# Optimization experiments

Hardware: AMD Instinct MI355X
Metric: run time of the kernel (lower is better)

Reference implementation:

```python
import math
import jax, jax.numpy as jnp
import numpy as np

T_STEPS = 65536
T_S = 1.0      # net_params['t_s']
THETA = 10.0   # net_params['af_params']['theta']


def _eps_func(mult, tau, epsilon, t_end, t_s):
    vals = []
    for t in np.arange(0, t_end, t_s):
        v = mult * t / tau * math.exp(1 - t / tau)
        if abs(v) < abs(epsilon) and t > tau:
            break
        vals.append(v)
    return vals


def _srm_kernel(mult, tau, epsilon, t_end, t_s):
    # replicates SlayerTrainer._calculate_srm_kernel: pad-to-odd, prepend zeros, flip
    k = _eps_func(mult, tau, epsilon, t_end, t_s)
    if len(k) % 2 == 0:
        k.append(0.0)
    k = np.asarray(k, dtype=np.float32)
    k = np.concatenate([np.zeros(len(k) - 1, np.float32), k])[::-1].copy()
    return k  # (K,), K odd; causal after cross-correlation with pad K//2


def setup_inputs() -> dict:
    key = jax.random.key(0)
    k1, k2, k3 = jax.random.split(key, 3)
    x = jax.random.uniform(k1, (1, 1, 1, 250, T_STEPS), jnp.float32)
    srm = jnp.asarray(_srm_kernel(1.0, 10.0, 1e-4, 200, T_S))                 # sr_params
    ref = jnp.asarray(np.asarray(_eps_func(-20.0, 1.0, 1e-4, 200, T_S), np.float32))  # ref_params
    # SpikeLinear weights, init N(0, std=weights_init)
    w1 = jax.random.normal(k2, (25, 250), jnp.float32) * 4.0
    w2 = jax.random.normal(k3, (1, 25), jnp.float32) * 4.0
    return {"x": x, "srm": srm, "ref": ref, "w1": w1, "w2": w2}


def srm_conv(z, srm):
    # z: (C, T). Per-channel 1-D cross-correlation with 'same' padding,
    # equal to F.conv3d(x, eye-SRM kernel, padding=(0,0,K//2)) * t_s.
    K = srm.shape[0]
    p = K // 2
    lhs = z[:, None, :]            # (C, 1, T) -- channels as batch
    rhs = srm[None, None, :]       # (1, 1, K)
    out = jax.lax.conv_general_dilated(
        lhs, rhs, window_strides=(1,), padding=[(p, p)],
        dimension_numbers=("NCW", "OIW", "NCW"))
    return out[:, 0, :] * T_S


def gen_spikes(pot, ref):
    # Sequential integrate-fire with refractory feedback (slayer_cuda.get_spikes_cuda).
    # pot: (C, T). Carry = per-neuron buffer of scheduled future refractory additions.
    C = pot.shape[0]
    L = ref.shape[0]
    # ref[j] is added to potentials[t+j] on a spike at t (ref[0]==0); after the
    # shift, buf[0] corresponds to time t+1, so schedule ref[1:].
    ref_next = jnp.concatenate([ref[1:], jnp.zeros((1,), pot.dtype)])

    def step(buf, p_t):
        u = p_t + buf[:, 0]                           # membrane incl. refractory
        s = (u >= THETA).astype(pot.dtype)
        buf = jnp.concatenate([buf[:, 1:], jnp.zeros((C, 1), pot.dtype)], axis=1)
        buf = buf + s[:, None] * ref_next[None, :]
        return buf, (u, s / T_S)

    buf0 = jnp.zeros((C, L), pot.dtype)
    _, (u_seq, s_seq) = jax.lax.scan(step, buf0, pot.T)
    return u_seq.T, s_seq.T  # (C, T), (C, T)


def reference(x, srm, ref, w1, w2):
    h = srm_conv(x[0, 0, 0], srm)        # (250, T) SRM-filtered input spikes
    h = w1 @ h                           # (25, T)  SpikeLinear fc1
    _, s1 = gen_spikes(h, ref)           # (25, T)  spikes layer 1
    h = srm_conv(s1, srm)                # (25, T)  SRM on hidden spikes
    h = w2 @ h                           # (1, T)   SpikeLinear fc2
    _, s2 = gen_spikes(h, ref)           # (1, T)
    return s2.reshape(1, 1, 1, 1, -1)
```

## Files before the change

### kernel.cpp

```cpp
#include <hip/hip_runtime.h>


#define T_LEN   65536
#define NCH     250
#define NO1     25
#define KTAPS   129
#define PAD     128
#define SRM_LEN 257
#define REF_LEN 16
#define THETA_F 10.0f
#define LBLK    128
#define NBK     512
#define WARM    128
#define TT      128
#define FTILE   1024
#define FT2     1024
#define NWORDS  (T_LEN / 32)
#define NGRP    16

__device__ __forceinline__ void srm_step(float p, const float (&rn)[15], float (&b)[15],
                                         unsigned &m, float &sf_out) {
  float u = p + b[0];
  unsigned sp = (u >= THETA_F) ? 1u : 0u;
  float sf = sp ? 1.0f : 0.0f;
#pragma unroll
  for (int j = 0; j < 14; ++j) b[j] = __builtin_fmaf(sf, rn[j], b[j + 1]);
  b[14] = __fmul_rn(sf, rn[14]);
  m = (m << 1) | sp;
  sf_out = sf;
}

__global__ void k_fill(float* out, float v) {
  out[blockIdx.x * 256 + threadIdx.x] = v;
}

__global__ __launch_bounds__(1024, 4) void k_mm1(const float* __restrict__ x,
                                                 const float* __restrict__ w1,
                                                 float* __restrict__ y1t) {
  __shared__ __align__(16) float part[NGRP][5][TT];
  const int tid = threadIdx.x;
  const int lane = tid & 63;
  const int wv = __builtin_amdgcn_readfirstlane(tid >> 6);
  const int t0 = blockIdx.x * TT;
  const int cs = wv * 15 + (wv < 10 ? wv : 10);
  const int cn = (wv < 10) ? 16 : 15;
  float acc[NO1][2];
#pragma unroll
  for (int o = 0; o < NO1; ++o) { acc[o][0] = 0.f; acc[o][1] = 0.f; }
  const float* xp = x + (size_t)cs * T_LEN + t0 + lane * 2;

  auto ld = [&](int ci) -> float2 {
    return (ci < cn) ? *(const float2*)(xp + (size_t)ci * T_LEN)
                     : make_float2(0.f, 0.f);
  };
  auto use = [&](int ci, float2 xv) {
    if (ci < cn) {
#pragma unroll
      for (int o = 0; o < NO1; ++o) {
        float wvv = w1[o * NCH + cs + ci];
        acc[o][0] = __builtin_fmaf(wvv, xv.x, acc[o][0]);
        acc[o][1] = __builtin_fmaf(wvv, xv.y, acc[o][1]);
      }
    }
  };

  float2 A0 = ld(0), A1 = ld(1), A2 = ld(2), A3 = ld(3);
  float2 B0, B1, B2, B3;
  for (int cb = 0; cb < cn; cb += 8) {
    B0 = ld(cb + 4); B1 = ld(cb + 5); B2 = ld(cb + 6); B3 = ld(cb + 7);
    use(cb + 0, A0); use(cb + 1, A1); use(cb + 2, A2); use(cb + 3, A3);
    A0 = ld(cb + 8); A1 = ld(cb + 9); A2 = ld(cb + 10); A3 = ld(cb + 11);
    use(cb + 4, B0); use(cb + 5, B1); use(cb + 6, B2); use(cb + 7, B3);
  }
  float* yb = y1t + (size_t)blockIdx.x * (NO1 * TT);
#pragma unroll
  for (int r = 0; r < 5; ++r) {
#pragma unroll
    for (int oo = 0; oo < 5; ++oo) {
      int o = r * 5 + oo;
      *(float2*)&part[wv][oo][lane * 2] = make_float2(acc[o][0], acc[o][1]);
    }
    __syncthreads();
    if (tid < 5 * (TT / 4)) {
      int oo = tid >> 5;
      int p4 = (tid & 31) * 4;
      float4 s = *(const float4*)&part[0][oo][p4];
#pragma unroll
      for (int g = 1; g < NGRP; ++g) {
        float4 p = *(const float4*)&part[g][oo][p4];
        s.x = __fadd_rn(s.x, p.x);
        s.y = __fadd_rn(s.y, p.y);
        s.z = __fadd_rn(s.z, p.z);
        s.w = __fadd_rn(s.w, p.w);
      }
      *(float4*)&yb[(r * 5 + oo) * TT + p4] = s;
    }
    __syncthreads();
  }
}

__global__ __launch_bounds__(256, 8) void k_fir1(const float* __restrict__ y1t,
                                                 const float* __restrict__ srm,
                                                 float* __restrict__ pot1) {
  __shared__ __align__(16) float win[FTILE + PAD];
  const int tid = threadIdx.x;
  const int o = blockIdx.y;
  const int t0 = blockIdx.x * FTILE;
  for (int j = tid; j < FTILE + PAD; j += 256) {
    int g = t0 - PAD + j;
    win[j] = (g >= 0)
        ? y1t[(size_t)(g >> 7) * (NO1 * TT) + o * TT + (g & (TT - 1))] : 0.0f;
  }
  __syncthreads();
  const int base = tid * 4;
  float q0 = 0.0f, q1 = 0.0f, q2 = 0.0f, q3 = 0.0f;
#pragma unroll
  for (int i = 32; i >= 0; --i) {
    float4 v = *(const float4*)&win[base + 4 * i];
#pragma unroll
    for (int l = 3; l >= 0; --l) {
      float vl = (l == 0) ? v.x : (l == 1) ? v.y : (l == 2) ? v.z : v.w;
#pragma unroll
      for (int k = 0; k < 4; ++k) {
        int d = 128 + k - 4 * i - l;
        if (d >= 0 && d <= 128) {
          float e = srm[4 * i + l - k];
          if (k == 0) q0 = __builtin_fmaf(e, vl, q0);
          else if (k == 1) q1 = __builtin_fmaf(e, vl, q1);
          else if (k == 2) q2 = __builtin_fmaf(e, vl, q2);
          else q3 = __builtin_fmaf(e, vl, q3);
        }
      }
    }
  }
  *(float4*)&pot1[(size_t)o * T_LEN + t0 + base] = make_float4(q0, q1, q2, q3);
}

__global__ __launch_bounds__(256) void k_pot2(const unsigned* __restrict__ s1p,
                                              const float* __restrict__ srm,
                                              const float* __restrict__ w2,
                                              float* __restrict__ pot2) {
  __shared__ __align__(16) float zs[FT2 + PAD];
  const int tid = threadIdx.x;
  const int t0 = blockIdx.x * FT2;
  for (int j = tid; j < FT2 + PAD; j += 256) {
    int g = t0 - PAD + j;
    float z = 0.0f;
    if (g >= 0) {
      int wi = g >> 5, sh = g & 31;
#pragma unroll
      for (int o = 0; o < NO1; ++o) {
        unsigned wvv = s1p[o * NWORDS + wi];
        z += ((wvv >> sh) & 1u) ? w2[o] : 0.0f;
      }
    }
    zs[j] = z;
  }
  __syncthreads();
  const int base = tid * 4;
  float q0 = 0.0f, q1 = 0.0f, q2 = 0.0f, q3 = 0.0f;
#pragma unroll
  for (int i = 32; i >= 0; --i) {
    float4 v = *(const float4*)&zs[base + 4 * i];
#pragma unroll
    for (int l = 3; l >= 0; --l) {
      float vl = (l == 0) ? v.x : (l == 1) ? v.y : (l == 2) ? v.z : v.w;
#pragma unroll
      for (int k = 0; k < 4; ++k) {
        int d = 128 + k - 4 * i - l;
        if (d >= 0 && d <= 128) {
          float e = srm[4 * i + l - k];
          if (k == 0) q0 = __builtin_fmaf(e, vl, q0);
          else if (k == 1) q1 = __builtin_fmaf(e, vl, q1);
          else if (k == 2) q2 = __builtin_fmaf(e, vl, q2);
          else q3 = __builtin_fmaf(e, vl, q3);
        }
      }
    }
  }
  *(float4*)&pot2[t0 + base] = make_float4(q0, q1, q2, q3);
}

template <int C, bool PACKED>
__global__ __launch_bounds__(64) void k_scan_spec(const float* __restrict__ pot,
                                                  const float* __restrict__ refk,
                                                  float* __restrict__ s,
                                                  unsigned* __restrict__ sp_,
                                                  unsigned* __restrict__ specin_m,
                                                  unsigned* __restrict__ specout_m,
                                                  float* __restrict__ specout_b) {
  int idx = blockIdx.x * 64 + threadIdx.x;
  if (idx >= C * NBK) return;
  int c = idx / NBK;
  int bb = idx - c * NBK;
  int tsr = bb * LBLK - WARM;
  float rn[15];
#pragma unroll
  for (int j = 0; j < 15; ++j) rn[j] = refk[j + 1];
  float b[15];
#pragma unroll
  for (int j = 0; j < 15; ++j) b[j] = 0.0f;
  unsigned m = 0;
  const float* prow = pot + (size_t)c * T_LEN;
  float* srow = PACKED ? nullptr : (s + (size_t)c * T_LEN);
  unsigned* srowp = PACKED ? (sp_ + (size_t)c * NWORDS) : nullptr;

  auto proc4 = [&](float4 pv, int tg, bool emit) {
    float s0, s1v, s2, s3;
    srm_step(pv.x, rn, b, m, s0);
    srm_step(pv.y, rn, b, m, s1v);
    srm_step(pv.z, rn, b, m, s2);
    srm_step(pv.w, rn, b, m, s3);
    if (emit) {
      if (PACKED) {
        if (((tg + 3) & 31) == 31) srowp[(tg - 28) >> 5] = __brev(m);
      } else {
        *(float4*)(srow + tg) = make_float4(s0, s1v, s2, s3);
      }
    }
  };

  for (int k = 0; k < WARM + LBLK; k += 16) {
    if (k == WARM) specin_m[idx] = m & 0x7FFFu;
    int t = tsr + k;
    if (t < 0) continue;
    float4 p0 = *(const float4*)(prow + t);
    float4 p1 = *(const float4*)(prow + t + 4);
    float4 p2 = *(const float4*)(prow + t + 8);
    float4 p3 = *(const float4*)(prow + t + 12);
    const bool emit = (k >= WARM);
    proc4(p0, t, emit);
    proc4(p1, t + 4, emit);
    proc4(p2, t + 8, emit);
    proc4(p3, t + 12, emit);
  }
  specout_m[idx] = m & 0x7FFFu;
#pragma unroll
  for (int j = 0; j < 15; ++j) specout_b[idx * 16 + j] = b[j];
}

template <int C, bool PACKED>
__global__ __launch_bounds__(64) void k_scan_fix(const float* __restrict__ pot,
                                                 const float* __restrict__ refk,
                                                 float* __restrict__ s,
                                                 unsigned* __restrict__ sp_,
                                                 const unsigned* __restrict__ specin_m,
                                                 const unsigned* __restrict__ specout_m,
                                                 const float* __restrict__ specout_b) {
  const int c = blockIdx.x;
  const int lane = threadIdx.x;
  float rn[15];
#pragma unroll
  for (int j = 0; j < 15; ++j) rn[j] = refk[j + 1];
  float b[15];
#pragma unroll
  for (int j = 0; j < 15; ++j) b[j] = 0.0f;
  unsigned m = 0;
  bool haveB = true;
  const float* prow = pot + (size_t)c * T_LEN;
  float* srow = PACKED ? nullptr : (s + (size_t)c * T_LEN);
  unsigned* srowp = PACKED ? (sp_ + (size_t)c * NWORDS) : nullptr;
  unsigned prev_last = 0;

  unsigned siv[NBK / 64], sov[NBK / 64];
#pragma unroll
  for (int g = 0; g < NBK / 64; ++g) {
    siv[g] = specin_m[c * NBK + g * 64 + lane];
    sov[g] = specout_m[c * NBK + g * 64 + lane];
  }
#pragma unroll
  for (int g = 0; g < NBK / 64; ++g) {
    const unsigned si = siv[g];
    const unsigned so = sov[g];
    unsigned so_prev = __shfl_up(so, 1);
    if (lane == 0) so_prev = prev_last;
    const unsigned long long flags = __ballot(si == so_prev);
    prev_last = __shfl(so, 63);
    const unsigned si0 = __shfl(si, 0);
    if (flags == ~0ull && (m & 0x7FFFu) == si0) {
      m = prev_last;
      haveB = false;
      continue;
    }
    for (int r = 0; r < 64; ++r) {
      const unsigned sir = __shfl(si, r);
      const unsigned sor = __shfl(so, r);
      if ((m & 0x7FFFu) == sir) {
        m = sor;
        haveB = false;
      } else {
        const int bbr = g * 64 + r;
        if (!haveB) {
          const int pb = (c * NBK + bbr - 1) * 16;
#pragma unroll
          for (int q2 = 0; q2 < 15; ++q2) b[q2] = specout_b[pb + q2];
          haveB = true;
        }
        const int t0 = bbr * LBLK;
        for (int t = t0; t < t0 + LBLK; t += 4) {
          float4 pv = *(const float4*)(prow + t);
          float s0, s1v, s2, s3;
          srm_step(pv.x, rn, b, m, s0);
          srm_step(pv.y, rn, b, m, s1v);
          srm_step(pv.z, rn, b, m, s2);
          srm_step(pv.w, rn, b, m, s3);
          if (PACKED) {
            if ((((t + 3) & 31) == 31) && lane == 0) srowp[(t - 28) >> 5] = __brev(m);
          } else {
            if (lane == 0) *(float4*)(srow + t) = make_float4(s0, s1v, s2, s3);
          }
        }
        haveB = true;
      }
    }
  }
}

extern "C" void kernel_launch(void* const* d_in, const int* in_sizes, int n_in,
                              void* d_out, int out_size, void* d_ws, size_t ws_size,
                              hipStream_t stream) {
  const float* x    = (const float*)d_in[0];
  const float* srm  = (const float*)d_in[1];
  const float* refk = (const float*)d_in[2];
  const float* w1   = (const float*)d_in[3];
  const float* w2   = (const float*)d_in[4];
  float* out = (float*)d_out;

  float bad = 0.0f;
  if (n_in != 5) bad = 3.0f;
  else if (in_sizes[0] != NCH * T_LEN) bad = 4.0f;
  else if (in_sizes[1] != SRM_LEN)     bad = 5.0f;
  else if (in_sizes[2] != REF_LEN)     bad = 6.0f;
  else if (in_sizes[3] != NO1 * NCH)   bad = 7.0f;
  else if (in_sizes[4] != NO1)         bad = 8.0f;
  else if (out_size != T_LEN)          bad = 9.0f;
  if (bad != 0.0f) {
    k_fill<<<T_LEN / 256, 256, 0, stream>>>(out, bad);
    return;
  }

  size_t off = 0;
  auto alloc = [&](size_t bytes) { size_t o = off; off = (off + bytes + 255) & ~(size_t)255; return o; };
  char* ws = (char*)d_ws;
  size_t oY1  = alloc((size_t)NO1 * T_LEN * 4);
  size_t oP1  = alloc((size_t)NO1 * T_LEN * 4);
  size_t oS1P = alloc((size_t)NO1 * NWORDS * 4);
  size_t oP2  = alloc((size_t)T_LEN * 4);
  if (ws_size < off) {
    k_fill<<<T_LEN / 256, 256, 0, stream>>>(out, 2.0f);
    return;
  }

  float*    y1t  = (float*)(ws + oY1);
  float*    pot1 = (float*)(ws + oP1);
  unsigned* s1p  = (unsigned*)(ws + oS1P);
  float*    pot2 = (float*)(ws + oP2);
  char* yb = ws + oY1;
  unsigned* si1 = (unsigned*)(yb);
  unsigned* so1 = (unsigned*)(yb + 51200);
  float*    sb1 = (float*)   (yb + 102400);
  unsigned* si2 = (unsigned*)(yb + 921600);
  unsigned* so2 = (unsigned*)(yb + 923648);
  float*    sb2 = (float*)   (yb + 925696);

  k_mm1<<<T_LEN / TT, 1024, 0, stream>>>(x, w1, y1t);
  k_fir1<<<dim3(T_LEN / FTILE, NO1), 256, 0, stream>>>(y1t, srm, pot1);
  k_scan_spec<NO1, true><<<(NO1 * NBK + 63) / 64, 64, 0, stream>>>(
      pot1, refk, nullptr, s1p, si1, so1, sb1);
  k_scan_fix<NO1, true><<<NO1, 64, 0, stream>>>(pot1, refk, nullptr, s1p, si1, so1, sb1);
  k_pot2<<<T_LEN / FT2, 256, 0, stream>>>(s1p, srm, w2, pot2);
  k_scan_spec<1, false><<<(NBK + 63) / 64, 64, 0, stream>>>(
      pot2, refk, out, nullptr, si2, so2, sb2);
  k_scan_fix<1, false><<<1, 64, 0, stream>>>(pot2, refk, out, nullptr, si2, so2, sb2);
}
```

Before: 98.65 us.

## Repack fc1 weights per wave group and halve mm1 block size with full unrolling

New measurement: 94.43 us. 4.3% less time.

```diff
diff --git a/kernel.cpp b/kernel.cpp
--- a/kernel.cpp
+++ b/kernel.cpp
@@ -16,7 +16,7 @@
 #define FTILE   1024
 #define FT2     1024
 #define NWORDS  (T_LEN / 32)
-#define NGRP    16
+#define NGRP    8
 
 __device__ __forceinline__ void srm_step(float p, const float (&rn)[15], float (&b)[15],
                                          unsigned &m, float &sf_out) {
@@ -34,44 +34,75 @@
   out[blockIdx.x * 256 + threadIdx.x] = v;
 }
 
-__global__ __launch_bounds__(1024, 4) void k_mm1(const float* __restrict__ x,
-                                                 const float* __restrict__ w1,
-                                                 float* __restrict__ y1t) {
+__global__ __launch_bounds__(256) void k_prep2(const float* __restrict__ w1,
+                                               float* __restrict__ wg) {
+  for (int i = threadIdx.x; i < NGRP * 32 * NO1; i += 256) {
+    int g = i / (32 * NO1);
+    int r = i - g * 32 * NO1;
+    int ci = r / NO1;
+    int o = r - ci * NO1;
+    int cs = g * 31 + (g < 2 ? g : 2);
+    int cn = (g < 2) ? 32 : 31;
+    wg[i] = (ci < cn) ? w1[o * NCH + cs + ci] : 0.0f;
+  }
+}
+
+template <int CI>
+__device__ __forceinline__ void use_slot(const float* __restrict__ wgp,
+                                         float (&acc)[NO1][2], float2 xv) {
+#pragma unroll
+  for (int o = 0; o < NO1; ++o) {
+    float wvv = wgp[CI * NO1 + o];
+    acc[o][0] = __builtin_fmaf(wvv, xv.x, acc[o][0]);
+    acc[o][1] = __builtin_fmaf(wvv, xv.y, acc[o][1]);
+  }
+}
+
+__global__ __launch_bounds__(512, 6) void k_mm1(const float* __restrict__ x,
+                                                const float* __restrict__ wg,
+                                                float* __restrict__ y1t) {
   __shared__ __align__(16) float part[NGRP][5][TT];
   const int tid = threadIdx.x;
   const int lane = tid & 63;
   const int wv = __builtin_amdgcn_readfirstlane(tid >> 6);
   const int t0 = blockIdx.x * TT;
-  const int cs = wv * 15 + (wv < 10 ? wv : 10);
-  const int cn = (wv < 10) ? 16 : 15;
+  const int cs = wv * 31 + (wv < 2 ? wv : 2);
+  const int cn = (wv < 2) ? 32 : 31;
+  const int s31 = cn - 1;
+  const float* wgp = wg + wv * (32 * NO1);
+  const float* xp = x + (size_t)cs * T_LEN + t0 + lane * 2;
   float acc[NO1][2];
 #pragma unroll
   for (int o = 0; o < NO1; ++o) { acc[o][0] = 0.f; acc[o][1] = 0.f; }
-  const float* xp = x + (size_t)cs * T_LEN + t0 + lane * 2;
-
-  auto ld = [&](int ci) -> float2 {
-    return (ci < cn) ? *(const float2*)(xp + (size_t)ci * T_LEN)
-                     : make_float2(0.f, 0.f);
-  };
-  auto use = [&](int ci, float2 xv) {
-    if (ci < cn) {
-#pragma unroll
-      for (int o = 0; o < NO1; ++o) {
-        float wvv = w1[o * NCH + cs + ci];
-        acc[o][0] = __builtin_fmaf(wvv, xv.x, acc[o][0]);
-        acc[o][1] = __builtin_fmaf(wvv, xv.y, acc[o][1]);
-      }
-    }
-  };
-
-  float2 A0 = ld(0), A1 = ld(1), A2 = ld(2), A3 = ld(3);
-  float2 B0, B1, B2, B3;
-  for (int cb = 0; cb < cn; cb += 8) {
-    B0 = ld(cb + 4); B1 = ld(cb + 5); B2 = ld(cb + 6); B3 = ld(cb + 7);
-    use(cb + 0, A0); use(cb + 1, A1); use(cb + 2, A2); use(cb + 3, A3);
-    A0 = ld(cb + 8); A1 = ld(cb + 9); A2 = ld(cb + 10); A3 = ld(cb + 11);
-    use(cb + 4, B0); use(cb + 5, B1); use(cb + 6, B2); use(cb + 7, B3);
-  }
+
+#define LDX(ci) (*(const float2*)(xp + (size_t)(ci) * T_LEN))
+  float2 A0, A1, A2, A3, B0, B1, B2, B3;
+  A0 = LDX(0);  A1 = LDX(1);  A2 = LDX(2);  A3 = LDX(3);
+  B0 = LDX(4);  B1 = LDX(5);  B2 = LDX(6);  B3 = LDX(7);
+  use_slot<0>(wgp, acc, A0);  use_slot<1>(wgp, acc, A1);
+  use_slot<2>(wgp, acc, A2);  use_slot<3>(wgp, acc, A3);
+  A0 = LDX(8);  A1 = LDX(9);  A2 = LDX(10); A3 = LDX(11);
+  use_slot<4>(wgp, acc, B0);  use_slot<5>(wgp, acc, B1);
+  use_slot<6>(wgp, acc, B2);  use_slot<7>(wgp, acc, B3);
+  B0 = LDX(12); B1 = LDX(13); B2 = LDX(14); B3 = LDX(15);
+  use_slot<8>(wgp, acc, A0);  use_slot<9>(wgp, acc, A1);
+  use_slot<10>(wgp, acc, A2); use_slot<11>(wgp, acc, A3);
+  A0 = LDX(16); A1 = LDX(17); A2 = LDX(18); A3 = LDX(19);
+  use_slot<12>(wgp, acc, B0); use_slot<13>(wgp, acc, B1);
+  use_slot<14>(wgp, acc, B2); use_slot<15>(wgp, acc, B3);
+  B0 = LDX(20); B1 = LDX(21); B2 = LDX(22); B3 = LDX(23);
+  use_slot<16>(wgp, acc, A0); use_slot<17>(wgp, acc, A1);
+  use_slot<18>(wgp, acc, A2); use_slot<19>(wgp, acc, A3);
+  A0 = LDX(24); A1 = LDX(25); A2 = LDX(26); A3 = LDX(27);
+  use_slot<20>(wgp, acc, B0); use_slot<21>(wgp, acc, B1);
+  use_slot<22>(wgp, acc, B2); use_slot<23>(wgp, acc, B3);
+  B0 = LDX(28); B1 = LDX(29); B2 = LDX(30); B3 = LDX(s31);
+  use_slot<24>(wgp, acc, A0); use_slot<25>(wgp, acc, A1);
+  use_slot<26>(wgp, acc, A2); use_slot<27>(wgp, acc, A3);
+  use_slot<28>(wgp, acc, B0); use_slot<29>(wgp, acc, B1);
+  use_slot<30>(wgp, acc, B2); use_slot<31>(wgp, acc, B3);
+#undef LDX
+
   float* yb = y1t + (size_t)blockIdx.x * (NO1 * TT);
 #pragma unroll
   for (int r = 0; r < 5; ++r) {
@@ -346,6 +377,7 @@
   size_t oP1  = alloc((size_t)NO1 * T_LEN * 4);
   size_t oS1P = alloc((size_t)NO1 * NWORDS * 4);
   size_t oP2  = alloc((size_t)T_LEN * 4);
+  size_t oWG  = alloc((size_t)NGRP * 32 * NO1 * 4);
   if (ws_size < off) {
     k_fill<<<T_LEN / 256, 256, 0, stream>>>(out, 2.0f);
     return;
@@ -355,6 +387,7 @@
   float*    pot1 = (float*)(ws + oP1);
   unsigned* s1p  = (unsigned*)(ws + oS1P);
   float*    pot2 = (float*)(ws + oP2);
+  float*    wg   = (float*)(ws + oWG);
   char* yb = ws + oY1;
   unsigned* si1 = (unsigned*)(yb);
   unsigned* so1 = (unsigned*)(yb + 51200);
@@ -363,7 +396,8 @@
   unsigned* so2 = (unsigned*)(yb + 923648);
   float*    sb2 = (float*)   (yb + 925696);
 
-  k_mm1<<<T_LEN / TT, 1024, 0, stream>>>(x, w1, y1t);
+  k_prep2<<<1, 256, 0, stream>>>(w1, wg);
+  k_mm1<<<T_LEN / TT, 512, 0, stream>>>(x, wg, y1t);
   k_fir1<<<dim3(T_LEN / FTILE, NO1), 256, 0, stream>>>(y1t, srm, pot1);
   k_scan_spec<NO1, true><<<(NO1 * NBK + 63) / 64, 64, 0, stream>>>(
       pot1, refk, nullptr, s1p, si1, so1, sb1);
```

## Restructure fc1 matmul to stage x tile in LDS with per-wave output groups

Applied to the files above, without the earlier changes.

After: 136.8 us. 1.39x slower.

```diff
diff --git a/kernel.cpp b/kernel.cpp
--- a/kernel.cpp
+++ b/kernel.cpp
@@ -12,11 +12,10 @@
 #define LBLK    128
 #define NBK     512
 #define WARM    128
-#define TT      128
+#define TT      64
 #define FTILE   1024
-#define FT2     1024
+#define FT2     512
 #define NWORDS  (T_LEN / 32)
-#define NGRP    16
 
 __device__ __forceinline__ void srm_step(float p, const float (&rn)[15], float (&b)[15],
                                          unsigned &m, float &sf_out) {
@@ -34,82 +33,57 @@
   out[blockIdx.x * 256 + threadIdx.x] = v;
 }
 
-__global__ __launch_bounds__(1024, 4) void k_mm1(const float* __restrict__ x,
-                                                 const float* __restrict__ w1,
-                                                 float* __restrict__ y1t) {
-  __shared__ __align__(16) float part[NGRP][5][TT];
+__global__ __launch_bounds__(256) void k_prep(const float* __restrict__ w1,
+                                              float* __restrict__ wT) {
+  for (int i = threadIdx.x; i < NO1 * NCH; i += 256) {
+    int c = i / NO1, o = i - c * NO1;
+    wT[i] = w1[o * NCH + c];
+  }
+}
+
+__global__ __launch_bounds__(256) void k_mm1(const float* __restrict__ x,
+                                             const float* __restrict__ wT,
+                                             float* __restrict__ y1) {
+  __shared__ __align__(16) float xs[NCH][TT];
   const int tid = threadIdx.x;
-  const int lane = tid & 63;
-  const int wv = __builtin_amdgcn_readfirstlane(tid >> 6);
   const int t0 = blockIdx.x * TT;
-  const int cs = wv * 15 + (wv < 10 ? wv : 10);
-  const int cn = (wv < 10) ? 16 : 15;
-  float acc[NO1][2];
-#pragma unroll
-  for (int o = 0; o < NO1; ++o) { acc[o][0] = 0.f; acc[o][1] = 0.f; }
-  const float* xp = x + (size_t)cs * T_LEN + t0 + lane * 2;
-
-  auto ld = [&](int ci) -> float2 {
-    return (ci < cn) ? *(const float2*)(xp + (size_t)ci * T_LEN)
-                     : make_float2(0.f, 0.f);
-  };
-  auto use = [&](int ci, float2 xv) {
-    if (ci < cn) {
-#pragma unroll
-      for (int o = 0; o < NO1; ++o) {
-        float wvv = w1[o * NCH + cs + ci];
-        acc[o][0] = __builtin_fmaf(wvv, xv.x, acc[o][0]);
-        acc[o][1] = __builtin_fmaf(wvv, xv.y, acc[o][1]);
-      }
-    }
-  };
-
-  float2 A0 = ld(0), A1 = ld(1), A2 = ld(2), A3 = ld(3);
-  float2 B0, B1, B2, B3;
-  for (int cb = 0; cb < cn; cb += 8) {
-    B0 = ld(cb + 4); B1 = ld(cb + 5); B2 = ld(cb + 6); B3 = ld(cb + 7);
-    use(cb + 0, A0); use(cb + 1, A1); use(cb + 2, A2); use(cb + 3, A3);
-    A0 = ld(cb + 8); A1 = ld(cb + 9); A2 = ld(cb + 10); A3 = ld(cb + 11);
-    use(cb + 4, B0); use(cb + 5, B1); use(cb + 6, B2); use(cb + 7, B3);
-  }
-  float* yb = y1t + (size_t)blockIdx.x * (NO1 * TT);
-#pragma unroll
-  for (int r = 0; r < 5; ++r) {
-#pragma unroll
-    for (int oo = 0; oo < 5; ++oo) {
-      int o = r * 5 + oo;
-      *(float2*)&part[wv][oo][lane * 2] = make_float2(acc[o][0], acc[o][1]);
-    }
-    __syncthreads();
-    if (tid < 5 * (TT / 4)) {
-      int oo = tid >> 5;
-      int p4 = (tid & 31) * 4;
-      float4 s = *(const float4*)&part[0][oo][p4];
-#pragma unroll
-      for (int g = 1; g < NGRP; ++g) {
-        float4 p = *(const float4*)&part[g][oo][p4];
-        s.x = __fadd_rn(s.x, p.x);
-        s.y = __fadd_rn(s.y, p.y);
-        s.z = __fadd_rn(s.z, p.z);
-        s.w = __fadd_rn(s.w, p.w);
-      }
-      *(float4*)&yb[(r * 5 + oo) * TT + p4] = s;
-    }
-    __syncthreads();
-  }
-}
-
-__global__ __launch_bounds__(256, 8) void k_fir1(const float* __restrict__ y1t,
+  for (int j = tid; j < NCH * (TT / 4); j += 256) {
+    int row = j >> 4, col = (j & 15) * 4;
+    *(float4*)&xs[row][col] = *(const float4*)&x[(size_t)row * T_LEN + t0 + col];
+  }
+  __syncthreads();
+  const int p = tid & 63;
+  const int og = __builtin_amdgcn_readfirstlane(tid >> 6);
+  const int ob = og * 6;
+  const int no = (og == 3) ? 7 : 6;
+  float acc[7];
+#pragma unroll
+  for (int j = 0; j < 7; ++j) acc[j] = 0.f;
+  const float* wp = wT + ob;
+#pragma unroll 5
+  for (int c = 0; c < NCH; ++c) {
+    float xv = xs[c][p];
+    const float* wr = wp + c * NO1;
+#pragma unroll
+    for (int j = 0; j < 7; ++j)
+      acc[j] = __builtin_fmaf(wr[j], xv, acc[j]);
+  }
+#pragma unroll
+  for (int j = 0; j < 7; ++j)
+    if (j < no) y1[(size_t)(ob + j) * T_LEN + t0 + p] = acc[j];
+}
+
+__global__ __launch_bounds__(256, 8) void k_fir1(const float* __restrict__ y1,
                                                  const float* __restrict__ srm,
                                                  float* __restrict__ pot1) {
   __shared__ __align__(16) float win[FTILE + PAD];
   const int tid = threadIdx.x;
   const int o = blockIdx.y;
   const int t0 = blockIdx.x * FTILE;
+  const float* yr = y1 + (size_t)o * T_LEN;
   for (int j = tid; j < FTILE + PAD; j += 256) {
     int g = t0 - PAD + j;
-    win[j] = (g >= 0)
-        ? y1t[(size_t)(g >> 7) * (NO1 * TT) + o * TT + (g & (TT - 1))] : 0.0f;
+    win[j] = (g >= 0) ? yr[g] : 0.0f;
   }
   __syncthreads();
   const int base = tid * 4;
@@ -136,14 +110,14 @@
   *(float4*)&pot1[(size_t)o * T_LEN + t0 + base] = make_float4(q0, q1, q2, q3);
 }
 
-__global__ __launch_bounds__(256) void k_pot2(const unsigned* __restrict__ s1p,
+__global__ __launch_bounds__(128) void k_pot2(const unsigned* __restrict__ s1p,
                                               const float* __restrict__ srm,
                                               const float* __restrict__ w2,
                                               float* __restrict__ pot2) {
   __shared__ __align__(16) float zs[FT2 + PAD];
   const int tid = threadIdx.x;
   const int t0 = blockIdx.x * FT2;
-  for (int j = tid; j < FT2 + PAD; j += 256) {
+  for (int j = tid; j < FT2 + PAD; j += 128) {
     int g = t0 - PAD + j;
     float z = 0.0f;
     if (g >= 0) {
@@ -346,15 +320,17 @@
   size_t oP1  = alloc((size_t)NO1 * T_LEN * 4);
   size_t oS1P = alloc((size_t)NO1 * NWORDS * 4);
   size_t oP2  = alloc((size_t)T_LEN * 4);
+  size_t oWT  = alloc((size_t)NO1 * NCH * 4);
   if (ws_size < off) {
     k_fill<<<T_LEN / 256, 256, 0, stream>>>(out, 2.0f);
     return;
   }
 
-  float*    y1t  = (float*)(ws + oY1);
+  float*    y1   = (float*)(ws + oY1);
   float*    pot1 = (float*)(ws + oP1);
   unsigned* s1p  = (unsigned*)(ws + oS1P);
   float*    pot2 = (float*)(ws + oP2);
+  float*    wT   = (float*)(ws + oWT);
   char* yb = ws + oY1;
   unsigned* si1 = (unsigned*)(yb);
   unsigned* so1 = (unsigned*)(yb + 51200);
@@ -363,12 +339,13 @@
   unsigned* so2 = (unsigned*)(yb + 923648);
   float*    sb2 = (float*)   (yb + 925696);
 
-  k_mm1<<<T_LEN / TT, 1024, 0, stream>>>(x, w1, y1t);
-  k_fir1<<<dim3(T_LEN / FTILE, NO1), 256, 0, stream>>>(y1t, srm, pot1);
+  k_prep<<<1, 256, 0, stream>>>(w1, wT);
+  k_mm1<<<T_LEN / TT, 256, 0, stream>>>(x, wT, y1);
+  k_fir1<<<dim3(T_LEN / FTILE, NO1), 256, 0, stream>>>(y1, srm, pot1);
   k_scan_spec<NO1, true><<<(NO1 * NBK + 63) / 64, 64, 0, stream>>>(
       pot1, refk, nullptr, s1p, si1, so1, sb1);
   k_scan_fix<NO1, true><<<NO1, 64, 0, stream>>>(pot1, refk, nullptr, s1p, si1, so1, sb1);
-  k_pot2<<<T_LEN / FT2, 256, 0, stream>>>(s1p, srm, w2, pot2);
+  k_pot2<<<T_LEN / FT2, 128, 0, stream>>>(s1p, srm, w2, pot2);
   k_scan_spec<1, false><<<(NBK + 63) / 64, 64, 0, stream>>>(
       pot2, refk, out, nullptr, si2, so2, sb2);
   k_scan_fix<1, false><<<1, 64, 0, stream>>>(pot2, refk, out, nullptr, si2, so2, sb2);
```
